# Performance work log

Measured on AMD Instinct MI355X. Metric: run time of the kernel, lower is better.

The kernel has to match this reference:

```python
import jax, jax.numpy as jnp
import numpy as np
from jax import lax

IMG_H, IMG_W = 800, 800
FM_H, FM_W = 50, 50
SIZES = (32.0, 64.0, 128.0)
RATIOS = (0.5, 1.0, 2.0)
A = len(SIZES) * len(RATIOS)          # 9 anchors per location
PRE_NMS = 512
POST_NMS = 128
MIN_SCORE = 0.5
IOU_THRESH = 0.7
MIN_SIZE = 0.001


def gen_anchor_boxes():
    """Anchors in (x1,y1,x2,y2), location-major / anchor-minor ordering
    (matches the permute(0,2,1).reshape(-1,4) layout of the offsets)."""
    sy, sx = IMG_H / FM_H, IMG_W / FM_W
    cy = (np.arange(FM_H) + 0.5) * sy
    cx = (np.arange(FM_W) + 0.5) * sx
    whs = []
    for s in SIZES:
        for r in RATIOS:
            h = s * np.sqrt(r)
            w = s / np.sqrt(r)
            whs.append((w, h))
    whs = np.asarray(whs, np.float32)                      # [A,2]
    cyg, cxg = np.meshgrid(cy, cx, indexing='ij')          # [H,W]
    ctr = np.stack([cxg, cyg], -1)[:, :, None, :]          # [H,W,1,2] (cx,cy)
    half = whs[None, None] / 2.0                           # [1,1,A,2]
    boxes = np.concatenate([ctr - half, ctr + half], -1)   # [H,W,A,4]
    return jnp.asarray(boxes.reshape(-1, 4), jnp.float32)  # [H*W*A,4]


def conv2d(x, w, b, pad):
    y = lax.conv_general_dilated(x, w, (1, 1), [(pad, pad), (pad, pad)],
                                 dimension_numbers=('NCHW', 'OIHW', 'NCHW'))
    return y + b[None, :, None, None]


def decode_boxes(offsets, anchors):
    """offsets [B,N,4] = (dx,dy,dw,dh); anchors [N,4] corners -> corners."""
    aw = anchors[:, 2] - anchors[:, 0]
    ah = anchors[:, 3] - anchors[:, 1]
    acx = anchors[:, 0] + 0.5 * aw
    acy = anchors[:, 1] + 0.5 * ah
    px = acx + offsets[..., 0] * aw
    py = acy + offsets[..., 1] * ah
    pw = aw * jnp.exp(offsets[..., 2])
    ph = ah * jnp.exp(offsets[..., 3])
    return jnp.stack([px - 0.5 * pw, py - 0.5 * ph,
                      px + 0.5 * pw, py + 0.5 * ph], -1)


def proposals_one_image(boxes, scores):
    """boxes [N,4], scores [N] -> padded ([POST_NMS,4],[POST_NMS])."""
    s, idx = lax.top_k(scores, PRE_NMS)          # pre-NMS top-k (sorted desc)
    b = boxes[idx]                               # [PRE,4]
    b = jnp.stack([jnp.clip(b[:, 0], 0.0, IMG_W),
                   jnp.clip(b[:, 1], 0.0, IMG_H),
                   jnp.clip(b[:, 2], 0.0, IMG_W),
                   jnp.clip(b[:, 3], 0.0, IMG_H)], -1)
    w = b[:, 2] - b[:, 0]
    h = b[:, 3] - b[:, 1]
    valid = (w >= MIN_SIZE) & (h >= MIN_SIZE) & (s >= MIN_SCORE)
    # pairwise IoU (NMS decisions are discrete -> stop_gradient)
    bi = lax.stop_gradient(b)
    area = (bi[:, 2] - bi[:, 0]) * (bi[:, 3] - bi[:, 1])
    lt = jnp.maximum(bi[:, None, :2], bi[None, :, :2])
    rb = jnp.minimum(bi[:, None, 2:], bi[None, :, 2:])
    wh = jnp.clip(rb - lt, 0.0)
    inter = wh[..., 0] * wh[..., 1]
    iou = inter / (area[:, None] + area[None, :] - inter + 1e-9)
    rng = jnp.arange(PRE_NMS)

    def body(keep, i):
        sup = (iou[i] > IOU_THRESH) & (rng > i) & keep[i]
        return keep & ~sup, None

    keep, _ = lax.scan(body, valid, rng)         # greedy NMS over sorted cands
    masked = jnp.where(keep, s, -1.0)
    top_s, top_i = lax.top_k(masked, POST_NMS)   # kept boxes keep score order
    ok = top_s >= MIN_SCORE
    out_b = b[top_i] * ok[:, None].astype(b.dtype)
    out_s = jnp.where(ok, top_s, 0.0)
    return out_b, out_s


def rpn_forward(feature_maps, w1, b1, w2, b2, w3, b3):
    B = feature_maps.shape[0]
    shared = jax.nn.relu(conv2d(feature_maps, w1, b1, 1))      # [B,512,H,W]
    cls = jax.nn.sigmoid(conv2d(shared, w2, b2, 0))            # [B,A,H,W]
    off = conv2d(shared, w3, b3, 0)                            # [B,4A,H,W]
    # location-major, anchor-minor flattening (matches torch permute/reshape)
    scores = cls.reshape(B, A, -1).transpose(0, 2, 1).reshape(B, -1)        # [B,N]
    offsets = off.reshape(B, 4 * A, -1).transpose(0, 2, 1).reshape(B, -1, 4)
    anchors = gen_anchor_boxes()
    boxes = decode_boxes(offsets, anchors)                     # [B,N,4]
    return jax.vmap(proposals_one_image)(boxes, scores)        # padded outputs


def setup_inputs() -> dict:
    key = jax.random.key(0)
    ks = jax.random.split(key, 4)
    fm = jax.random.normal(ks[0], (16, 512, FM_H, FM_W), jnp.float32)
    w1 = jax.random.normal(ks[1], (512, 512, 3, 3), jnp.float32) * 0.02
    b1 = jnp.zeros((512,), jnp.float32)
    w2 = jax.random.normal(ks[2], (9, 512, 1, 1), jnp.float32) * 0.05
    b2 = jnp.zeros((9,), jnp.float32)
    w3 = jax.random.normal(ks[3], (36, 512, 1, 1), jnp.float32) * 0.01
    b3 = jnp.zeros((36,), jnp.float32)
    return {"feature_maps": fm, "w1": w1, "b1": b1, "w2": w2, "b2": b2,
            "w3": w3, "b3": b3}


def reference(feature_maps, w1, b1, w2, b2, w3, b3):
    return rpn_forward(feature_maps, w1, b1, w2, b2, w3, b3)
```

## Files before the change

### kernel.cpp

```cpp
#include <hip/hip_runtime.h>
#include <math.h>
#include <stdint.h>

#define FMW 50
#define P_IMG 2500
#define CIN 512
#define NANCH 22500
#define BATCH 16
#define PRE 512
#define POST 128
#define NCHUNK 44
#define NPAD (NCHUNK * 512)
#define MB 192
#define NTIL 14
#define WIN 320

typedef __attribute__((ext_vector_type(8))) short short8;
typedef __attribute__((ext_vector_type(16))) float f32x16;

union U4S8 { uint4 u; short8 s; };

__device__ __forceinline__ unsigned short f2bf(float x) {
    unsigned u = __float_as_uint(x);
    unsigned r = u + 0x7FFFu + ((u >> 16) & 1u);
    return (unsigned short)(r >> 16);
}
__device__ __forceinline__ float bf2f(unsigned short h) {
    return __uint_as_float(((unsigned)h) << 16);
}

__device__ __forceinline__ void gload_lds16(const void* g, void* l) {
    __builtin_amdgcn_global_load_lds(
        (const __attribute__((address_space(1))) void*)g,
        (__attribute__((address_space(3))) void*)l, 16, 0, 0);
}

__global__ void k_prepack(const float* __restrict__ w1, char* __restrict__ w1pack) {
    int t = blockIdx.x * 256 + threadIdx.x;
    int l = t & 63;
    int NT = (t >> 6) & 15;
    int c = (t >> 10) & 31;
    int pos = t >> 15;
    int oc = NT * 32 + (l & 31);
    unsigned short hv[8], lv[8];
#pragma unroll
    for (int j = 0; j < 8; ++j) {
        int ci = c * 16 + (l >> 5) * 8 + j;
        float x = w1[((size_t)oc * 512 + ci) * 9 + pos];
        unsigned short h = f2bf(x);
        hv[j] = h;
        lv[j] = f2bf(x - bf2f(h));
    }
    size_t base = ((size_t)((pos * 32 + c) * 16 + NT) * 2) * 1024 + (size_t)l * 16;
    uint4 hu, lu;
    hu.x = hv[0] | ((unsigned)hv[1] << 16); hu.y = hv[2] | ((unsigned)hv[3] << 16);
    hu.z = hv[4] | ((unsigned)hv[5] << 16); hu.w = hv[6] | ((unsigned)hv[7] << 16);
    lu.x = lv[0] | ((unsigned)lv[1] << 16); lu.y = lv[2] | ((unsigned)lv[3] << 16);
    lu.z = lv[4] | ((unsigned)lv[5] << 16); lu.w = lv[6] | ((unsigned)lv[7] << 16);
    *(uint4*)(w1pack + base) = hu;
    *(uint4*)(w1pack + base + 1024) = lu;
}

__global__ __launch_bounds__(512, 2)
void k_conv_mfma(const float* __restrict__ fm, const char* __restrict__ w1pack,
                 const float* __restrict__ b1, const float* __restrict__ w2,
                 const float* __restrict__ b2, const float* __restrict__ w3,
                 const float* __restrict__ b3,
                 float* __restrict__ off_ws, unsigned long long* __restrict__ keys) {
    __shared__ __align__(16) char smem[123392];

    const int t = threadIdx.x;
    const int l = t & 63;
    const int w = t >> 6;
    const int r = w >> 2;
    const int q = w & 3;
    const int img = blockIdx.x / NTIL;
    const int p0 = (blockIdx.x % NTIL) * MB;

    f32x16 acc[3][4];
#pragma unroll
    for (int mt = 0; mt < 3; ++mt)
#pragma unroll
        for (int nt = 0; nt < 4; ++nt)
#pragma unroll
            for (int g = 0; g < 16; ++g) acc[mt][nt][g] = 0.f;

    int xs[3];
#pragma unroll
    for (int mt = 0; mt < 3; ++mt) xs[mt] = (p0 + r * 96 + mt * 32 + (l & 31)) % FMW;

    const int arb = (64 + r * 96 + (l & 31)) * 32 + (l >> 5) * 16;
    const size_t img_base = (size_t)img * CIN * P_IMG;
    const int DPOS[9] = {-51, -50, -49, -1, 0, 1, 49, 50, 51};

    char* Abuf = smem;

    auto stageA = [&](int cc) {
#pragma unroll
        for (int i = 0; i < 3; ++i) {
            int flat = i * 512 + t;
            if (flat < 1280) {
                int qq = flat & 3;
                int pxl = flat >> 2;
                int pw = p0 - 64 + pxl;
                bool ok = (pw >= 0) && (pw < P_IMG);
                float v[4];
#pragma unroll
                for (int k = 0; k < 4; ++k)
                    v[k] = ok ? fm[img_base + (size_t)(cc * 16 + qq * 4 + k) * P_IMG + pw] : 0.f;
                unsigned short h[4], lo[4];
#pragma unroll
                for (int k = 0; k < 4; ++k) {
                    h[k] = f2bf(v[k]);
                    lo[k] = f2bf(v[k] - bf2f(h[k]));
                }
                uint2 hu, lu;
                hu.x = h[0] | ((unsigned)h[1] << 16);  hu.y = h[2] | ((unsigned)h[3] << 16);
                lu.x = lo[0] | ((unsigned)lo[1] << 16); lu.y = lo[2] | ((unsigned)lo[3] << 16);
                *(uint2*)(Abuf + pxl * 32 + qq * 8) = hu;
                *(uint2*)(Abuf + 10240 + pxl * 32 + qq * 8) = lu;
            }
        }
    };

    auto stageB = [&](int kk) {
        int c = kk / 9, pos = kk % 9;
        const char* src = w1pack + (size_t)(pos * 32 + c) * 32768;
        char* dst = smem + 20480 + (kk % 3) * 32768;
#pragma unroll
        for (int j = 0; j < 4; ++j) {
            int chunk = w * 4 + j;
            gload_lds16(src + chunk * 1024 + l * 16, dst + chunk * 1024);
        }
    };

    stageB(0);
    stageB(1);
    stageA(0);
    asm volatile("s_waitcnt vmcnt(0) lgkmcnt(0)" ::: "memory");
    __builtin_amdgcn_s_barrier();
    asm volatile("" ::: "memory");

    for (int kk = 0; kk < 288; ++kk) {
        const int c = kk / 9, pos = kk % 9;
        if (kk < 286) stageB(kk + 2);

        if (kk < 286)       asm volatile("s_waitcnt vmcnt(8)" ::: "memory");
        else if (kk == 286) asm volatile("s_waitcnt vmcnt(4)" ::: "memory");
        else                asm volatile("s_waitcnt vmcnt(0)" ::: "memory");
        __builtin_amdgcn_s_barrier();
        asm volatile("" ::: "memory");

        const int dpos = DPOS[pos];
        const int dx = pos % 3 - 1;
        U4S8 ah[3], al[3];
        const char* ap = Abuf + arb + dpos * 32;
#pragma unroll
        for (int mt = 0; mt < 3; ++mt) {
            ah[mt].u = *(const uint4*)(ap + mt * 1024);
            al[mt].u = *(const uint4*)(ap + 10240 + mt * 1024);
            bool xok = (dx == 0) || (dx < 0 ? (xs[mt] > 0) : (xs[mt] < FMW - 1));
            if (!xok) {
                ah[mt].u.x = 0; ah[mt].u.y = 0; ah[mt].u.z = 0; ah[mt].u.w = 0;
                al[mt].u.x = 0; al[mt].u.y = 0; al[mt].u.z = 0; al[mt].u.w = 0;
            }
        }
        const char* bp = smem + 20480 + (kk % 3) * 32768 + q * 8192 + l * 16;
        __builtin_amdgcn_s_setprio(1);
#pragma unroll
        for (int nt = 0; nt < 4; ++nt) {
            U4S8 bh, bl;
            bh.u = *(const uint4*)(bp + nt * 2048);
            bl.u = *(const uint4*)(bp + nt * 2048 + 1024);
#pragma unroll
            for (int mt = 0; mt < 3; ++mt) {
                acc[mt][nt] = __builtin_amdgcn_mfma_f32_32x32x16_bf16(ah[mt].s, bh.s, acc[mt][nt], 0, 0, 0);
                acc[mt][nt] = __builtin_amdgcn_mfma_f32_32x32x16_bf16(al[mt].s, bh.s, acc[mt][nt], 0, 0, 0);
                acc[mt][nt] = __builtin_amdgcn_mfma_f32_32x32x16_bf16(ah[mt].s, bl.s, acc[mt][nt], 0, 0, 0);
            }
        }
        __builtin_amdgcn_s_setprio(0);

        if (pos == 8 && c < 31) {
            asm volatile("" ::: "memory");
            __builtin_amdgcn_s_barrier();
            asm volatile("" ::: "memory");
            stageA(c + 1);
            asm volatile("s_waitcnt lgkmcnt(0)" ::: "memory");
        }

        asm volatile("" ::: "memory");
        __builtin_amdgcn_s_barrier();
        asm volatile("" ::: "memory");
    }

    float* SH = (float*)smem;
    float* W  = (float*)(smem + 98816);
    float b1v[4];
#pragma unroll
    for (int nt = 0; nt < 4; ++nt) b1v[nt] = b1[q * 128 + nt * 32 + (l & 31)];

    const int pxe = t % 192;
    const int og = t / 192;
    const int no = (og == 0) ? 23 : 22;
    float p45[23];
#pragma unroll
    for (int m = 0; m < 23; ++m) p45[m] = 0.f;

    for (int rr = 0; rr < 4; ++rr) {
        __syncthreads();
#pragma unroll
        for (int i = 0; i < 12; ++i) {
            int e = i * 512 + t;
            if (e < 5760) {
                int o = e >> 7, cl = e & 127;
                W[o * 128 + cl] = (o < 9) ? w2[o * 512 + rr * 128 + cl]
                                          : w3[(o - 9) * 512 + rr * 128 + cl];
            }
        }
        if (q == rr) {
#pragma unroll
            for (int nt = 0; nt < 4; ++nt) {
                int oc_l = nt * 32 + (l & 31);
#pragma unroll
                for (int mt = 0; mt < 3; ++mt)
#pragma unroll
                    for (int g = 0; g < 16; ++g) {
                        int row = (g & 3) + 8 * (g >> 2) + 4 * (l >> 5);
                        SH[oc_l * 193 + r * 96 + mt * 32 + row] =
                            fmaxf(acc[mt][nt][g] + b1v[nt], 0.f);
                    }
            }
        }
        __syncthreads();
        if (og < 2) {
            for (int cl = 0; cl < 128; ++cl) {
                float sv = SH[cl * 193 + pxe];
#pragma unroll
                for (int m = 0; m < 23; ++m)
                    if (m < no) p45[m] = fmaf(sv, W[(og * 23 + m) * 128 + cl], p45[m]);
            }
        }
    }

    const int pE = p0 + pxe;
    if (og < 2 && pE < P_IMG) {
        for (int m = 0; m < no; ++m) {
            int o = og * 23 + m;
            if (o < 9) {
                float z = p45[m] + b2[o];
                float s = (z >= 0.f) ? (1.f / (1.f + expf(-z)))
                                     : (expf(z) / (1.f + expf(z)));
                unsigned n = (unsigned)(pE * 9 + o);
                unsigned long long key =
                    ((unsigned long long)__float_as_uint(s) << 32) |
                    (unsigned long long)(0xFFFFFFFFu - n);
                keys[(size_t)img * NPAD + n] = key;
            } else {
                int cc = o - 9;
                off_ws[((size_t)img * P_IMG + pE) * 36 + cc] = p45[m] + b3[cc];
            }
        }
    }
}

__global__ __launch_bounds__(256)
void k_sort_chunks(unsigned long long* __restrict__ keys) {
    __shared__ unsigned long long sk[512];
    const int t = threadIdx.x;
    const int img = blockIdx.x / NCHUNK;
    const int ch = blockIdx.x % NCHUNK;
    const size_t base = (size_t)img * NPAD + ch * 512;
    int a0 = ch * 512 + t, a1 = ch * 512 + t + 256;
    sk[t] = (a0 < NANCH) ? keys[base + t] : 0ull;
    sk[t + 256] = (a1 < NANCH) ? keys[base + t + 256] : 0ull;
    for (int k = 2; k <= 512; k <<= 1)
        for (int j = k >> 1; j > 0; j >>= 1) {
            __syncthreads();
            for (int i = t; i < 512; i += 256) {
                int lx = i ^ j;
                if (lx > i) {
                    unsigned long long a = sk[i], b = sk[lx];
                    bool desc = ((i & k) == 0);
                    if (desc ? (a < b) : (a > b)) { sk[i] = b; sk[lx] = a; }
                }
            }
        }
    __syncthreads();
    keys[base + t] = sk[t];
    keys[base + t + 256] = sk[t + 256];
}

__global__ __launch_bounds__(256)
void k_nms(const unsigned long long* __restrict__ keys,
           const float* __restrict__ off_ws, float* __restrict__ out) {
    __shared__ unsigned long long top[512];
    __shared__ unsigned long long chk[512];
    __shared__ float bx1[512], by1[512], bx2[512], by2[512], bar[512], bsc[512];
    __shared__ int keep[512];

    const int t = threadIdx.x;
    const int img = blockIdx.x;
    const size_t kbase = (size_t)img * NPAD;

    top[t] = keys[kbase + t];
    top[t + 256] = keys[kbase + t + 256];

    for (int c = 1; c < NCHUNK; ++c) {
        __syncthreads();
        chk[t] = keys[kbase + c * 512 + t];
        chk[t + 256] = keys[kbase + c * 512 + t + 256];
        __syncthreads();
        for (int i = t; i < 512; i += 256) {
            unsigned long long a = top[i], b = chk[511 - i];
            top[i] = (a > b) ? a : b;
        }
        for (int j = 256; j > 0; j >>= 1) {
            __syncthreads();
            int i = ((t & ~(j - 1)) << 1) | (t & (j - 1));
            unsigned long long a = top[i], b = top[i + j];
            if (a < b) { top[i] = b; top[i + j] = a; }
        }
    }
    __syncthreads();

    for (int i = t; i < 512; i += 256) {
        unsigned long long key = top[i];
        float s = __uint_as_float((unsigned)(key >> 32));
        unsigned id = 0xFFFFFFFFu - (unsigned)(key & 0xFFFFFFFFull);
        float x1 = 0.f, y1 = 0.f, x2 = 0.f, y2 = 0.f;
        bool valid = false;
        if (key != 0ull && id < (unsigned)NANCH) {
            int p = id / 9, a = id - p * 9;
            int gy = p / FMW, gx = p - gy * FMW;
            const double SS[3] = {32.0, 64.0, 128.0};
            const double RR[3] = {0.5, 1.0, 2.0};
            double sq = sqrt(RR[a % 3]);
            float wa32 = (float)(SS[a / 3] / sq);
            float ha32 = (float)(SS[a / 3] * sq);
            double cx = ((double)gx + 0.5) * 16.0;
            double cy = ((double)gy + 0.5) * 16.0;
            float ax1 = (float)(cx - (double)(wa32 * 0.5f));
            float ay1 = (float)(cy - (double)(ha32 * 0.5f));
            float ax2 = (float)(cx + (double)(wa32 * 0.5f));
            float ay2 = (float)(cy + (double)(ha32 * 0.5f));
            float aw = ax2 - ax1, ah2 = ay2 - ay1;
            float acx = ax1 + 0.5f * aw, acy = ay1 + 0.5f * ah2;
            const float4 off = *(const float4*)(off_ws + ((size_t)img * P_IMG + p) * 36 + a * 4);
            float px = acx + off.x * aw;
            float py = acy + off.y * ah2;
            float pw = aw * expf(off.z);
            float ph = ah2 * expf(off.w);
            x1 = fminf(fmaxf(px - 0.5f * pw, 0.f), 800.f);
            y1 = fminf(fmaxf(py - 0.5f * ph, 0.f), 800.f);
            x2 = fminf(fmaxf(px + 0.5f * pw, 0.f), 800.f);
            y2 = fminf(fmaxf(py + 0.5f * ph, 0.f), 800.f);
            float ww = x2 - x1, hh = y2 - y1;
            valid = (ww >= 1e-3f) && (hh >= 1e-3f) && (s >= 0.5f);
        }
        bx1[i] = x1; by1[i] = y1; bx2[i] = x2; by2[i] = y2;
        bar[i] = (x2 - x1) * (y2 - y1);
        bsc[i] = s;
        keep[i] = valid ? 1 : 0;
    }
    __syncthreads();

    for (int i = 0; i < PRE - 1; ++i) {
        __syncthreads();
        if (keep[i] == 0) continue;
        float xi1 = bx1[i], yi1 = by1[i], xi2 = bx2[i], yi2 = by2[i], ai = bar[i];
        for (int j = i + 1 + t; j < PRE; j += 256) {
            if (keep[j]) {
                float lx = fmaxf(xi1, bx1[j]);
                float ly = fmaxf(yi1, by1[j]);
                float rx = fminf(xi2, bx2[j]);
                float ry = fminf(yi2, by2[j]);
                float iw = fmaxf(rx - lx, 0.f);
                float ih = fmaxf(ry - ly, 0.f);
                float inter = iw * ih;
                float iou = inter / (ai + bar[j] - inter + 1e-9f);
                if (iou > 0.7f) keep[j] = 0;
            }
        }
    }
    __syncthreads();

    for (int i = t; i < 512; i += 256) {
        float m = keep[i] ? bsc[i] : -1.0f;
        unsigned u = __float_as_uint(m);
        u = (u & 0x80000000u) ? ~u : (u | 0x80000000u);
        chk[i] = ((unsigned long long)u << 32) | (unsigned long long)(511 - i);
    }
    for (int k = 2; k <= 512; k <<= 1)
        for (int j = k >> 1; j > 0; j >>= 1) {
            __syncthreads();
            for (int i = t; i < 512; i += 256) {
                int lx = i ^ j;
                if (lx > i) {
                    unsigned long long a = chk[i], b = chk[lx];
                    bool desc = ((i & k) == 0);
                    if (desc ? (a < b) : (a > b)) { chk[i] = b; chk[lx] = a; }
                }
            }
        }
    __syncthreads();

    if (t < POST) {
        unsigned long long key = chk[t];
        int slot = 511 - (int)(key & 0xFFFFFFFFull);
        float m = keep[slot] ? bsc[slot] : -1.0f;
        bool ok = (m >= 0.5f);
        float* ob = out + ((size_t)img * POST + t) * 4;
        ob[0] = ok ? bx1[slot] : 0.f;
        ob[1] = ok ? by1[slot] : 0.f;
        ob[2] = ok ? bx2[slot] : 0.f;
        ob[3] = ok ? by2[slot] : 0.f;
        out[(size_t)BATCH * POST * 4 + img * POST + t] = ok ? m : 0.f;
    }
}

extern "C" void kernel_launch(void* const* d_in, const int* in_sizes, int n_in,
                              void* d_out, int out_size, void* d_ws, size_t ws_size,
                              hipStream_t stream) {
    const float* fm = (const float*)d_in[0];
    const float* w1 = (const float*)d_in[1];
    const float* b1 = (const float*)d_in[2];
    const float* w2 = (const float*)d_in[3];
    const float* b2 = (const float*)d_in[4];
    const float* w3 = (const float*)d_in[5];
    const float* b3 = (const float*)d_in[6];
    float* out = (float*)d_out;

    char* ws = (char*)d_ws;
    char* w1pack = ws;
    float* off_ws = (float*)(ws + 0x900000);
    unsigned long long* keys = (unsigned long long*)(ws + 0xE80000);

    k_prepack<<<1152, 256, 0, stream>>>(w1, w1pack);
    k_conv_mfma<<<BATCH * NTIL, 512, 0, stream>>>(fm, w1pack, b1, w2, b2, w3, b3, off_ws, keys);
    k_sort_chunks<<<BATCH * NCHUNK, 256, 0, stream>>>(keys);
    k_nms<<<BATCH, 256, 0, stream>>>(keys, off_ws, out);
}
```

Before: 1.141 ms.

## Load conv weights directly into registers with double buffering instead of LDS staging

```diff
diff --git a/kernel.cpp b/kernel.cpp
--- a/kernel.cpp
+++ b/kernel.cpp
@@ -29,12 +29,6 @@
     return __uint_as_float(((unsigned)h) << 16);
 }
 
-__device__ __forceinline__ void gload_lds16(const void* g, void* l) {
-    __builtin_amdgcn_global_load_lds(
-        (const __attribute__((address_space(1))) void*)g,
-        (__attribute__((address_space(3))) void*)l, 16, 0, 0);
-}
-
 __global__ void k_prepack(const float* __restrict__ w1, char* __restrict__ w1pack) {
     int t = blockIdx.x * 256 + threadIdx.x;
     int l = t & 63;
@@ -123,34 +117,18 @@
         }
     };
 
-    auto stageB = [&](int kk) {
-        int c = kk / 9, pos = kk % 9;
-        const char* src = w1pack + (size_t)(pos * 32 + c) * 32768;
-        char* dst = smem + 20480 + (kk % 3) * 32768;
-#pragma unroll
-        for (int j = 0; j < 4; ++j) {
-            int chunk = w * 4 + j;
-            gload_lds16(src + chunk * 1024 + l * 16, dst + chunk * 1024);
+    const char* wq = w1pack + q * 8192 + (size_t)l * 16;
+    auto loadB = [&](int kk, uint4* bh, uint4* bl) {
+        const char* src = wq + (size_t)((kk % 9) * 32 + (kk / 9)) * 32768;
+#pragma unroll
+        for (int nt = 0; nt < 4; ++nt) {
+            bh[nt] = *(const uint4*)(src + nt * 2048);
+            bl[nt] = *(const uint4*)(src + nt * 2048 + 1024);
         }
     };
 
-    stageB(0);
-    stageB(1);
-    stageA(0);
-    asm volatile("s_waitcnt vmcnt(0) lgkmcnt(0)" ::: "memory");
-    __builtin_amdgcn_s_barrier();
-    asm volatile("" ::: "memory");
-
-    for (int kk = 0; kk < 288; ++kk) {
-        const int c = kk / 9, pos = kk % 9;
-        if (kk < 286) stageB(kk + 2);
-
-        if (kk < 286)       asm volatile("s_waitcnt vmcnt(8)" ::: "memory");
-        else if (kk == 286) asm volatile("s_waitcnt vmcnt(4)" ::: "memory");
-        else                asm volatile("s_waitcnt vmcnt(0)" ::: "memory");
-        __builtin_amdgcn_s_barrier();
-        asm volatile("" ::: "memory");
-
+    auto compute = [&](int kk, const uint4* bh4, const uint4* bl4) {
+        const int pos = kk % 9;
         const int dpos = DPOS[pos];
         const int dx = pos % 3 - 1;
         U4S8 ah[3], al[3];
@@ -165,13 +143,12 @@
                 al[mt].u.x = 0; al[mt].u.y = 0; al[mt].u.z = 0; al[mt].u.w = 0;
             }
         }
-        const char* bp = smem + 20480 + (kk % 3) * 32768 + q * 8192 + l * 16;
         __builtin_amdgcn_s_setprio(1);
 #pragma unroll
         for (int nt = 0; nt < 4; ++nt) {
             U4S8 bh, bl;
-            bh.u = *(const uint4*)(bp + nt * 2048);
-            bl.u = *(const uint4*)(bp + nt * 2048 + 1024);
+            bh.u = bh4[nt];
+            bl.u = bl4[nt];
 #pragma unroll
             for (int mt = 0; mt < 3; ++mt) {
                 acc[mt][nt] = __builtin_amdgcn_mfma_f32_32x32x16_bf16(ah[mt].s, bh.s, acc[mt][nt], 0, 0, 0);
@@ -180,18 +157,34 @@
             }
         }
         __builtin_amdgcn_s_setprio(0);
-
+    };
+
+    auto maybeStageA = [&](int kk) {
+        const int c = kk / 9, pos = kk % 9;
         if (pos == 8 && c < 31) {
             asm volatile("" ::: "memory");
             __builtin_amdgcn_s_barrier();
             asm volatile("" ::: "memory");
             stageA(c + 1);
             asm volatile("s_waitcnt lgkmcnt(0)" ::: "memory");
-        }
-
-        asm volatile("" ::: "memory");
-        __builtin_amdgcn_s_barrier();
-        asm volatile("" ::: "memory");
+            __builtin_amdgcn_s_barrier();
+            asm volatile("" ::: "memory");
+        }
+    };
+
+    uint4 bAh[4], bAl[4], bBh[4], bBl[4];
+    stageA(0);
+    loadB(0, bAh, bAl);
+    __syncthreads();
+
+    for (int kp = 0; kp < 144; ++kp) {
+        const int kk0 = kp * 2;
+        loadB(kk0 + 1, bBh, bBl);
+        compute(kk0, bAh, bAl);
+        maybeStageA(kk0);
+        if (kp < 143) loadB(kk0 + 2, bAh, bAl);
+        compute(kk0 + 1, bBh, bBl);
+        maybeStageA(kk0 + 1);
     }
 
     float* SH = (float*)smem;
```

After: 1.960 ms. +71.7%, slower.

## Use a single barrier per K-step and issue weight prefetch after it

Applied to the files above, without the earlier changes.

```diff
diff --git a/kernel.cpp b/kernel.cpp
--- a/kernel.cpp
+++ b/kernel.cpp
@@ -91,7 +91,6 @@
 
     const int arb = (64 + r * 96 + (l & 31)) * 32 + (l >> 5) * 16;
     const size_t img_base = (size_t)img * CIN * P_IMG;
-    const int DPOS[9] = {-51, -50, -49, -1, 0, 1, 49, 50, 51};
 
     char* Abuf = smem;
 
@@ -123,10 +122,10 @@
         }
     };
 
-    auto stageB = [&](int kk) {
+    auto stageB = [&](int kk, int bidx) {
         int c = kk / 9, pos = kk % 9;
         const char* src = w1pack + (size_t)(pos * 32 + c) * 32768;
-        char* dst = smem + 20480 + (kk % 3) * 32768;
+        char* dst = smem + 20480 + bidx * 32768;
 #pragma unroll
         for (int j = 0; j < 4; ++j) {
             int chunk = w * 4 + j;
@@ -134,27 +133,35 @@
         }
     };
 
-    stageB(0);
-    stageB(1);
+    stageB(0, 0);
+    stageB(1, 1);
     stageA(0);
-    asm volatile("s_waitcnt vmcnt(0) lgkmcnt(0)" ::: "memory");
-    __builtin_amdgcn_s_barrier();
-    asm volatile("" ::: "memory");
-
+    asm volatile("s_waitcnt lgkmcnt(0)" ::: "memory");
+
+    int c = 0, pos = 0;
+    int bcur = 0;
     for (int kk = 0; kk < 288; ++kk) {
-        const int c = kk / 9, pos = kk % 9;
-        if (kk < 286) stageB(kk + 2);
-
-        if (kk < 286)       asm volatile("s_waitcnt vmcnt(8)" ::: "memory");
-        else if (kk == 286) asm volatile("s_waitcnt vmcnt(4)" ::: "memory");
-        else                asm volatile("s_waitcnt vmcnt(0)" ::: "memory");
+        if (kk < 287) asm volatile("s_waitcnt vmcnt(4)" ::: "memory");
+        else          asm volatile("s_waitcnt vmcnt(0)" ::: "memory");
         __builtin_amdgcn_s_barrier();
         asm volatile("" ::: "memory");
 
-        const int dpos = DPOS[pos];
+        if (pos == 0 && c > 0) {
+            stageA(c);
+            asm volatile("s_waitcnt lgkmcnt(0)" ::: "memory");
+            __builtin_amdgcn_s_barrier();
+            asm volatile("" ::: "memory");
+        }
+
+        if (kk < 286) {
+            int sb = bcur + 2; if (sb >= 3) sb -= 3;
+            stageB(kk + 2, sb);
+        }
+
         const int dx = pos % 3 - 1;
+        const int dposv = (pos / 3 - 1) * FMW + dx;
         U4S8 ah[3], al[3];
-        const char* ap = Abuf + arb + dpos * 32;
+        const char* ap = Abuf + arb + dposv * 32;
 #pragma unroll
         for (int mt = 0; mt < 3; ++mt) {
             ah[mt].u = *(const uint4*)(ap + mt * 1024);
@@ -165,7 +172,7 @@
                 al[mt].u.x = 0; al[mt].u.y = 0; al[mt].u.z = 0; al[mt].u.w = 0;
             }
         }
-        const char* bp = smem + 20480 + (kk % 3) * 32768 + q * 8192 + l * 16;
+        const char* bp = smem + 20480 + bcur * 32768 + q * 8192 + l * 16;
         __builtin_amdgcn_s_setprio(1);
 #pragma unroll
         for (int nt = 0; nt < 4; ++nt) {
@@ -181,18 +188,13 @@
         }
         __builtin_amdgcn_s_setprio(0);
 
-        if (pos == 8 && c < 31) {
-            asm volatile("" ::: "memory");
-            __builtin_amdgcn_s_barrier();
-            asm volatile("" ::: "memory");
-            stageA(c + 1);
-            asm volatile("s_waitcnt lgkmcnt(0)" ::: "memory");
-        }
-
-        asm volatile("" ::: "memory");
-        __builtin_amdgcn_s_barrier();
-        asm volatile("" ::: "memory");
-    }
+        if (++pos == 9) { pos = 0; ++c; }
+        if (++bcur == 3) bcur = 0;
+    }
+
+    asm volatile("" ::: "memory");
+    __builtin_amdgcn_s_barrier();
+    asm volatile("" ::: "memory");
 
     float* SH = (float*)smem;
     float* W  = (float*)(smem + 98816);
```

New measurement: 1.134 ms. About the same (-0.6%).
